# Performance work log

Hardware: AMD Instinct MI355X
Metric: run time of the kernel (lower is better)

## Reference

```python
import jax, jax.numpy as jnp
import numpy as np

B, T = 16384, 79
DIMS = [(1, 64), (64, 32), (32, 16), (16, 8), (8, 16), (16, 32), (32, 64), (64, 79)]


def _simple_rnn(x, Wx, Wh, b, act, return_seq):
    # x: [B, T, D] -> SimpleRNN: h_t = act(x_t @ Wx + h_{t-1} @ Wh + b)
    xb = jnp.einsum('btd,du->btu', x, Wx) + b  # precompute input projection
    h0 = jnp.zeros((x.shape[0], Wh.shape[0]), x.dtype)

    def step(h, xt):
        h = act(xt + h @ Wh)
        return h, h

    hT, hs = jax.lax.scan(step, h0, jnp.swapaxes(xb, 0, 1))  # scan over time
    return jnp.swapaxes(hs, 0, 1) if return_seq else hT


def setup_inputs() -> dict:
    key = jax.random.key(0)
    ks = jax.random.split(key, 3 * len(DIMS) + 1)
    inp = {"x": jax.random.normal(ks[0], (B, T), dtype=jnp.float32)}
    for i, (d, u) in enumerate(DIMS):
        inp[f"Wx{i}"] = jax.random.normal(ks[1 + 3 * i], (d, u), dtype=jnp.float32) / np.sqrt(d).astype(np.float32)
        inp[f"Wh{i}"] = jax.random.normal(ks[2 + 3 * i], (u, u), dtype=jnp.float32) / np.sqrt(u).astype(np.float32)
        inp[f"b{i}"] = jnp.zeros((u,), dtype=jnp.float32)
    return inp


def reference(x, Wx0, Wh0, b0, Wx1, Wh1, b1, Wx2, Wh2, b2, Wx3, Wh3, b3,
              Wx4, Wh4, b4, Wx5, Wh5, b5, Wx6, Wh6, b6, Wx7, Wh7, b7):
    params = [(Wx0, Wh0, b0), (Wx1, Wh1, b1), (Wx2, Wh2, b2), (Wx3, Wh3, b3),
              (Wx4, Wh4, b4), (Wx5, Wh5, b5), (Wx6, Wh6, b6), (Wx7, Wh7, b7)]
    h = x[..., None]  # [B, T, 1]  (tf.expand_dims(x, -1))
    n = len(params)
    for i, (Wx, Wh, b) in enumerate(params):
        last = i == n - 1
        act = jax.nn.sigmoid if last else jax.nn.relu
        h = _simple_rnn(h, Wx, Wh, b, act, return_seq=not last)
    return h  # decoded: [B, 79]
```

## Files before the change

kernel.cpp:

```cpp
#include <hip/hip_runtime.h>
#include <hip/hip_bf16.h>

#define DEVFN static __device__ __forceinline__

typedef short bf16x8 __attribute__((ext_vector_type(8)));
typedef float f32x4  __attribute__((ext_vector_type(4)));

constexpr int TSEQ  = 79;
constexpr int NSTEP = TSEQ + 7;
constexpr int MWG   = 16;
constexpr int ROWU  = 344;
constexpr int NBLK  = 16384 / MWG;

constexpr int LD[8]   = {1,64,32,16,8,16,32,64};
constexpr int LU[8]   = {64,32,16,8,16,32,64,79};
constexpr int LS[8]   = {0,8,72,104,120,128,144,176};
constexpr int LO[8]   = {8,72,104,120,128,144,176,240};
constexpr int LKP[8]  = {96,96,64,32,32,64,96,160};
constexpr int LKS[8]  = {3,3,2,1,1,2,3,5};
constexpr int LUP[8]  = {64,32,16,16,16,32,64,80};
constexpr int WOFF[8] = {0,6144,9216,10240,10752,11264,13312,19456};
constexpr int WTOTAL  = 32256;

constexpr int WNG[4]     = {1,2,4,2};
constexpr int WGL[4][4]  = {{7,0,0,0},{7,1,0,0},{0,2,3,4},{6,5,0,0}};
constexpr int WGT0[4][4] = {{0,0,0,0},{3,0,0,0},{0,0,0,0},{0,0,0,0}};
constexpr int WGNT[4][4] = {{3,0,0,0},{2,2,0,0},{4,1,1,1},{4,2,0,0}};

DEVFN unsigned short f2bf(float f) {
  unsigned int u = __builtin_bit_cast(unsigned int, f);
  return (unsigned short)((u + 0x7FFFu + ((u >> 16) & 1u)) >> 16);
}
DEVFN unsigned int pk_rna(float a, float b) {
  unsigned int ua = __builtin_bit_cast(unsigned int, a) + 0x8000u;
  unsigned int ub = __builtin_bit_cast(unsigned int, b) + 0x8000u;
  return __builtin_amdgcn_perm(ub, ua, 0x07060302u);
}
DEVFN float sigmoidf(float v) {
  return __builtin_amdgcn_rcpf(1.0f + __expf(-v));
}

__global__ void __launch_bounds__(256) prep_weights(
    const float* Wx0, const float* Wh0, const float* Wx1, const float* Wh1,
    const float* Wx2, const float* Wh2, const float* Wx3, const float* Wh3,
    const float* Wx4, const float* Wh4, const float* Wx5, const float* Wh5,
    const float* Wx6, const float* Wh6, const float* Wx7, const float* Wh7,
    unsigned short* __restrict__ wt)
{
  const float* wxp[8] = {Wx0,Wx1,Wx2,Wx3,Wx4,Wx5,Wx6,Wx7};
  const float* whp[8] = {Wh0,Wh1,Wh2,Wh3,Wh4,Wh5,Wh6,Wh7};
  int idx = blockIdx.x * 256 + threadIdx.x;
  if (idx >= WTOTAL) return;
#pragma unroll
  for (int l = 0; l < 8; ++l) {
    int sz = LUP[l] * LKP[l];
    if (idx >= WOFF[l] && idx < WOFF[l] + sz) {
      int local = idx - WOFF[l];
      int j = local / LKP[l];
      int k = local - j * LKP[l];
      float v = 0.f;
      if (j < LU[l]) {
        if (l == 0) {
          if (k == 0) v = Wx0[j];
          else if (k >= 8 && k < 72) v = Wh0[(k - 8) * 64 + j];
        } else {
          if (k < LD[l]) v = wxp[l][k * LU[l] + j];
          else if (k < LD[l] + LU[l]) v = whp[l][(k - LD[l]) * LU[l] + j];
        }
      }
      wt[idx] = f2bf(v);
    }
  }
}

template <int W>
DEVFN void preload(const unsigned short* __restrict__ wt,
                   const float* const (&bptr)[8], int lane,
                   bf16x8 (&af)[16], f32x4 (&bi)[7])
{
  const int m0 = lane & 15, quad = lane >> 4;
  int ai = 0, ti = 0;
#pragma unroll
  for (int g = 0; g < 4; ++g) {
    if (g >= WNG[W]) break;
    const int l = WGL[W][g], t0 = WGT0[W][g], nt = WGNT[W][g];
    const int ks = LKS[l], Kp = LKP[l], u = LU[l];
#pragma unroll
    for (int t = 0; t < 4; ++t) {
      if (t >= nt) continue;
      const int j = (t0 + t) * 16 + m0;
      const unsigned short* base = wt + WOFF[l] + j * Kp;
#pragma unroll
      for (int k = 0; k < 5; ++k) {
        if (k >= ks) continue;
        af[ai + t * ks + k] = *reinterpret_cast<const bf16x8*>(base + k * 32 + quad * 8);
      }
      const float* bp = bptr[l];
      f32x4 bv;
#pragma unroll
      for (int r = 0; r < 4; ++r) {
        int j2 = (t0 + t) * 16 + quad * 4 + r;
        bv[r] = (j2 < u) ? bp[j2] : 0.0f;
      }
      bi[ti + t] = bv;
    }
    ai += nt * ks; ti += nt;
  }
}

template <int W>
DEVFN void step(int s, const unsigned short (&rb)[MWG][ROWU], unsigned short (&wb)[MWG][ROWU],
                const bf16x8 (&af)[16], const f32x4 (&bi)[7],
                const unsigned short (*xl)[80], float* __restrict__ out,
                int bb, int lane)
{
  const int m = lane & 15, quad = lane >> 4;
  int ai = 0, ti = 0;
#pragma unroll
  for (int g = 0; g < 4; ++g) {
    if (g >= WNG[W]) break;
    const int l = WGL[W][g], t0 = WGT0[W][g], nt = WGNT[W][g];
    const int ks = LKS[l], S = LS[l], O = LO[l], u = LU[l];
    if (s >= l && s <= l + TSEQ - 1) {
      f32x4 acc[4];
#pragma unroll
      for (int k = 0; k < 5; ++k) {
        if (k >= ks) break;
        bf16x8 bfv = *reinterpret_cast<const bf16x8*>(&rb[m][S + k * 32 + quad * 8]);
#pragma unroll
        for (int t = 0; t < 4; ++t)
          if (t < nt)
            acc[t] = __builtin_amdgcn_mfma_f32_16x16x32_bf16(
                af[ai + t * ks + k], bfv, (k == 0) ? bi[ti + t] : acc[t], 0, 0, 0);
      }
#pragma unroll
      for (int t = 0; t < 4; ++t) {
        if (t >= nt) continue;
        const int jb = (t0 + t) * 16 + quad * 4;
        float v0 = acc[t][0], v1 = acc[t][1], v2 = acc[t][2], v3 = acc[t][3];
        if (l == 7) {
          v0 = sigmoidf(v0); v1 = sigmoidf(v1); v2 = sigmoidf(v2); v3 = sigmoidf(v3);
          if (s == NSTEP - 1) {
            float* op = out + (size_t)(bb + m) * 79 + jb;
            if (jb + 0 < 79) op[0] = v0;
            if (jb + 1 < 79) op[1] = v1;
            if (jb + 2 < 79) op[2] = v2;
            if (jb + 3 < 79) op[3] = v3;
          } else {
            uint2 pk;
            pk.x = pk_rna(v0, v1);
            pk.y = pk_rna(v2, v3);
            *reinterpret_cast<uint2*>(&wb[m][O + jb]) = pk;
          }
        } else {
          if (jb < u) {
            v0 = fmaxf(v0, 0.f); v1 = fmaxf(v1, 0.f); v2 = fmaxf(v2, 0.f); v3 = fmaxf(v3, 0.f);
            uint2 pk;
            pk.x = pk_rna(v0, v1);
            pk.y = pk_rna(v2, v3);
            *reinterpret_cast<uint2*>(&wb[m][O + jb]) = pk;
          }
        }
      }
    }
    ai += nt * ks; ti += nt;
  }
  if constexpr (W == 0) {
    if (lane < MWG && s < TSEQ - 1) {
      wb[lane][0] = xl[lane][s + 1];
    }
  }
}

__global__ void __launch_bounds__(256)
__attribute__((amdgpu_waves_per_eu(4, 4)))
__attribute__((amdgpu_num_vgpr(128)))
rnn_wavefront(
    const float* __restrict__ x, const unsigned short* __restrict__ wt,
    const float* b0, const float* b1, const float* b2, const float* b3,
    const float* b4, const float* b5, const float* b6, const float* b7,
    float* __restrict__ out)
{
  __shared__ __align__(16) unsigned short hb0[MWG][ROWU];
  __shared__ __align__(16) unsigned short hb1[MWG][ROWU];
  __shared__ __align__(4)  unsigned short xl[MWG][80];
  const int tid = threadIdx.x, lane = tid & 63, wid = tid >> 6;
  const int bb = blockIdx.x * MWG;
  const float* bptr[8] = {b0, b1, b2, b3, b4, b5, b6, b7};

  {
    unsigned int* p0 = (unsigned int*)&hb0[0][0];
    unsigned int* p1 = (unsigned int*)&hb1[0][0];
    constexpr int NW = MWG * ROWU / 2;
    for (int i = tid; i < NW; i += 256) { p0[i] = 0; p1[i] = 0; }
  }
  {
    const float* xb = x + (size_t)bb * TSEQ;
    for (int i = tid; i < MWG * TSEQ; i += 256) {
      int r = i / TSEQ, c = i - r * TSEQ;
      xl[r][c] = f2bf(xb[i]);
    }
  }
  __syncthreads();
  if (tid < MWG) hb0[tid][0] = xl[tid][0];

  bf16x8 af[16];
  f32x4  bi[7];
  if (wid == 0)      preload<0>(wt, bptr, lane, af, bi);
  else if (wid == 1) preload<1>(wt, bptr, lane, af, bi);
  else if (wid == 2) preload<2>(wt, bptr, lane, af, bi);
  else               preload<3>(wt, bptr, lane, af, bi);
  __syncthreads();

#pragma unroll 1
  for (int s = 0; s < NSTEP; s += 2) {
    if (wid == 0)      step<0>(s, hb0, hb1, af, bi, xl, out, bb, lane);
    else if (wid == 1) step<1>(s, hb0, hb1, af, bi, xl, out, bb, lane);
    else if (wid == 2) step<2>(s, hb0, hb1, af, bi, xl, out, bb, lane);
    else               step<3>(s, hb0, hb1, af, bi, xl, out, bb, lane);
    __syncthreads();
    if (wid == 0)      step<0>(s + 1, hb1, hb0, af, bi, xl, out, bb, lane);
    else if (wid == 1) step<1>(s + 1, hb1, hb0, af, bi, xl, out, bb, lane);
    else if (wid == 2) step<2>(s + 1, hb1, hb0, af, bi, xl, out, bb, lane);
    else               step<3>(s + 1, hb1, hb0, af, bi, xl, out, bb, lane);
    __syncthreads();
  }
}

extern "C" void kernel_launch(void* const* d_in, const int* in_sizes, int n_in,
                              void* d_out, int out_size, void* d_ws, size_t ws_size,
                              hipStream_t stream)
{
  const float* x = (const float*)d_in[0];
  const float* Wx[8]; const float* Wh[8]; const float* b[8];
  for (int i = 0; i < 8; ++i) {
    Wx[i] = (const float*)d_in[1 + 3 * i];
    Wh[i] = (const float*)d_in[2 + 3 * i];
    b[i]  = (const float*)d_in[3 + 3 * i];
  }
  unsigned short* wt = (unsigned short*)d_ws;

  prep_weights<<<(WTOTAL + 255) / 256, 256, 0, stream>>>(
      Wx[0], Wh[0], Wx[1], Wh[1], Wx[2], Wh[2], Wx[3], Wh[3],
      Wx[4], Wh[4], Wx[5], Wh[5], Wx[6], Wh[6], Wx[7], Wh[7], wt);

  rnn_wavefront<<<NBLK, 256, 0, stream>>>(
      x, wt, b[0], b[1], b[2], b[3], b[4], b[5], b[6], b[7], (float*)d_out);
}
```

Measured before the change: 206.3 us.

## Run all eight RNN layers per wave with register-resident weights

Replaces the layer-wavefront schedule, where four waves each owned some layers and synchronised through block barriers on double-buffered LDS, with a scheme where each wave processes a private 16-row batch tile through all eight layers sequentially per timestep. All layer weights (63 bf16x8 fragments) and biases stay in registers, and occupancy drops to one wave per EU. Intra-wave LDS fences replace __syncthreads, and hidden-state fragments from the previous step are preloaded before the layer chain. This removes barrier stalls and cross-wave dependencies but raises register pressure and lowers latency hiding from occupancy. The serial per-wave dependency chain across eight layers may also expose MFMA and LDS latency.

```diff
diff --git a/kernel.cpp b/kernel.cpp
--- a/kernel.cpp
+++ b/kernel.cpp
@@ -7,10 +7,9 @@
 typedef float f32x4  __attribute__((ext_vector_type(4)));
 
 constexpr int TSEQ  = 79;
-constexpr int NSTEP = TSEQ + 7;
 constexpr int MWG   = 16;
 constexpr int ROWU  = 344;
-constexpr int NBLK  = 16384 / MWG;
+constexpr int NBLK  = 16384 / 64;
 
 constexpr int LD[8]   = {1,64,32,16,8,16,32,64};
 constexpr int LU[8]   = {64,32,16,8,16,32,64,79};
@@ -22,10 +21,14 @@
 constexpr int WOFF[8] = {0,6144,9216,10240,10752,11264,13312,19456};
 constexpr int WTOTAL  = 32256;
 
-constexpr int WNG[4]     = {1,2,4,2};
-constexpr int WGL[4][4]  = {{7,0,0,0},{7,1,0,0},{0,2,3,4},{6,5,0,0}};
-constexpr int WGT0[4][4] = {{0,0,0,0},{3,0,0,0},{0,0,0,0},{0,0,0,0}};
-constexpr int WGNT[4][4] = {{3,0,0,0},{2,2,0,0},{4,1,1,1},{4,2,0,0}};
+constexpr int NT[8]  = {4,2,1,1,1,2,4,5};
+constexpr int AO[8]  = {0,12,18,20,21,22,26,38};
+constexpr int TO[8]  = {0,4,6,7,8,9,11,15};
+constexpr int NH[8]  = {3,1,1,0,0,1,2,3};
+constexpr int BHO[8] = {0,3,4,5,5,5,6,8};
+constexpr int KORD[8][5] = {
+  {0,1,2,0,0},{2,0,1,0,0},{1,0,0,0,0},{0,0,0,0,0},
+  {0,0,0,0,0},{1,0,0,0,0},{1,2,0,0,0},{2,3,4,0,1}};
 
 DEVFN unsigned short f2bf(float f) {
   unsigned int u = __builtin_bit_cast(unsigned int, f);
@@ -38,6 +41,12 @@
 }
 DEVFN float sigmoidf(float v) {
   return __builtin_amdgcn_rcpf(1.0f + __expf(-v));
+}
+
+DEVFN void ds_fence() {
+  __builtin_amdgcn_sched_barrier(0);
+  asm volatile("s_waitcnt lgkmcnt(0)" ::: "memory");
+  __builtin_amdgcn_sched_barrier(0);
 }
 
 __global__ void __launch_bounds__(256) prep_weights(
@@ -73,158 +82,170 @@
   }
 }
 
-template <int W>
-DEVFN void preload(const unsigned short* __restrict__ wt,
-                   const float* const (&bptr)[8], int lane,
-                   bf16x8 (&af)[16], f32x4 (&bi)[7])
+DEVFN void preload_all(const unsigned short* __restrict__ wt,
+                       const float* const (&bptr)[8], int lane,
+                       bf16x8 (&af)[63], f32x4 (&bi)[20])
 {
   const int m0 = lane & 15, quad = lane >> 4;
-  int ai = 0, ti = 0;
-#pragma unroll
-  for (int g = 0; g < 4; ++g) {
-    if (g >= WNG[W]) break;
-    const int l = WGL[W][g], t0 = WGT0[W][g], nt = WGNT[W][g];
-    const int ks = LKS[l], Kp = LKP[l], u = LU[l];
-#pragma unroll
-    for (int t = 0; t < 4; ++t) {
-      if (t >= nt) continue;
-      const int j = (t0 + t) * 16 + m0;
-      const unsigned short* base = wt + WOFF[l] + j * Kp;
+#pragma unroll
+  for (int l = 0; l < 8; ++l) {
+#pragma unroll
+    for (int t = 0; t < 5; ++t) {
+      if (t >= NT[l]) continue;
+      const unsigned short* base = wt + WOFF[l] + (t * 16 + m0) * LKP[l];
 #pragma unroll
       for (int k = 0; k < 5; ++k) {
-        if (k >= ks) continue;
-        af[ai + t * ks + k] = *reinterpret_cast<const bf16x8*>(base + k * 32 + quad * 8);
+        if (k >= LKS[l]) continue;
+        af[AO[l] + t * LKS[l] + k] =
+            *reinterpret_cast<const bf16x8*>(base + k * 32 + quad * 8);
       }
       const float* bp = bptr[l];
       f32x4 bv;
 #pragma unroll
       for (int r = 0; r < 4; ++r) {
-        int j2 = (t0 + t) * 16 + quad * 4 + r;
-        bv[r] = (j2 < u) ? bp[j2] : 0.0f;
-      }
-      bi[ti + t] = bv;
-    }
-    ai += nt * ks; ti += nt;
-  }
-}
-
-template <int W>
-DEVFN void step(int s, const unsigned short (&rb)[MWG][ROWU], unsigned short (&wb)[MWG][ROWU],
-                const bf16x8 (&af)[16], const f32x4 (&bi)[7],
-                const unsigned short (*xl)[80], float* __restrict__ out,
-                int bb, int lane)
+        int j2 = t * 16 + quad * 4 + r;
+        bv[r] = (j2 < LU[l]) ? bp[j2] : 0.0f;
+      }
+      bi[TO[l] + t] = bv;
+    }
+  }
+}
+
+template <int L, bool LAST>
+DEVFN void layer(const unsigned short* rbase,
+                 unsigned short* wbase,
+                 const bf16x8 (&af)[63], const f32x4 (&bi)[20],
+                 const bf16x8 (&bh)[11],
+                 float* __restrict__ out, int bb, int m, int quad)
+{
+  constexpr int ks = LKS[L], nt = NT[L], S = LS[L], O = LO[L], u = LU[L];
+  bf16x8 fr[5];
+#pragma unroll
+  for (int i = 0; i < 5; ++i) {
+    if (i < NH[L] || i >= ks) continue;
+    fr[i] = *reinterpret_cast<const bf16x8*>(rbase + S + KORD[L][i] * 32);
+  }
+  f32x4 acc[5];
+#pragma unroll
+  for (int i = 0; i < 5; ++i) {
+    if (i >= ks) continue;
+    bf16x8 b = (i < NH[L]) ? bh[BHO[L] + i] : fr[i];
+#pragma unroll
+    for (int t = 0; t < 5; ++t) {
+      if (t >= nt) continue;
+      acc[t] = __builtin_amdgcn_mfma_f32_16x16x32_bf16(
+          af[AO[L] + t * ks + KORD[L][i]], b,
+          (i == 0) ? bi[TO[L] + t] : acc[t], 0, 0, 0);
+    }
+  }
+#pragma unroll
+  for (int t = 0; t < 5; ++t) {
+    if (t >= nt) continue;
+    const int jb = t * 16 + quad * 4;
+    float v0 = acc[t][0], v1 = acc[t][1], v2 = acc[t][2], v3 = acc[t][3];
+    if (L == 7) {
+      v0 = sigmoidf(v0); v1 = sigmoidf(v1); v2 = sigmoidf(v2); v3 = sigmoidf(v3);
+      if (LAST) {
+        float* op = out + (size_t)(bb + m) * 79 + jb;
+        if (jb + 0 < 79) op[0] = v0;
+        if (jb + 1 < 79) op[1] = v1;
+        if (jb + 2 < 79) op[2] = v2;
+        if (jb + 3 < 79) op[3] = v3;
+      } else {
+        uint2 pk;
+        pk.x = pk_rna(v0, v1);
+        pk.y = pk_rna(v2, v3);
+        *reinterpret_cast<uint2*>(wbase + O + t * 16) = pk;
+      }
+    } else {
+      if (jb < u) {
+        v0 = fmaxf(v0, 0.f); v1 = fmaxf(v1, 0.f); v2 = fmaxf(v2, 0.f); v3 = fmaxf(v3, 0.f);
+        uint2 pk;
+        pk.x = pk_rna(v0, v1);
+        pk.y = pk_rna(v2, v3);
+        *reinterpret_cast<uint2*>(wbase + O + t * 16) = pk;
+      }
+    }
+  }
+}
+
+template <bool LAST>
+DEVFN void timestep(int t, unsigned short (&hw)[MWG][ROWU],
+                    const unsigned short (&xw)[MWG][80],
+                    const bf16x8 (&af)[63], const f32x4 (&bi)[20],
+                    float* __restrict__ out, int bb, int lane)
 {
   const int m = lane & 15, quad = lane >> 4;
-  int ai = 0, ti = 0;
-#pragma unroll
-  for (int g = 0; g < 4; ++g) {
-    if (g >= WNG[W]) break;
-    const int l = WGL[W][g], t0 = WGT0[W][g], nt = WGNT[W][g];
-    const int ks = LKS[l], S = LS[l], O = LO[l], u = LU[l];
-    if (s >= l && s <= l + TSEQ - 1) {
-      f32x4 acc[4];
-#pragma unroll
-      for (int k = 0; k < 5; ++k) {
-        if (k >= ks) break;
-        bf16x8 bfv = *reinterpret_cast<const bf16x8*>(&rb[m][S + k * 32 + quad * 8]);
-#pragma unroll
-        for (int t = 0; t < 4; ++t)
-          if (t < nt)
-            acc[t] = __builtin_amdgcn_mfma_f32_16x16x32_bf16(
-                af[ai + t * ks + k], bfv, (k == 0) ? bi[ti + t] : acc[t], 0, 0, 0);
-      }
-#pragma unroll
-      for (int t = 0; t < 4; ++t) {
-        if (t >= nt) continue;
-        const int jb = (t0 + t) * 16 + quad * 4;
-        float v0 = acc[t][0], v1 = acc[t][1], v2 = acc[t][2], v3 = acc[t][3];
-        if (l == 7) {
-          v0 = sigmoidf(v0); v1 = sigmoidf(v1); v2 = sigmoidf(v2); v3 = sigmoidf(v3);
-          if (s == NSTEP - 1) {
-            float* op = out + (size_t)(bb + m) * 79 + jb;
-            if (jb + 0 < 79) op[0] = v0;
-            if (jb + 1 < 79) op[1] = v1;
-            if (jb + 2 < 79) op[2] = v2;
-            if (jb + 3 < 79) op[3] = v3;
-          } else {
-            uint2 pk;
-            pk.x = pk_rna(v0, v1);
-            pk.y = pk_rna(v2, v3);
-            *reinterpret_cast<uint2*>(&wb[m][O + jb]) = pk;
-          }
-        } else {
-          if (jb < u) {
-            v0 = fmaxf(v0, 0.f); v1 = fmaxf(v1, 0.f); v2 = fmaxf(v2, 0.f); v3 = fmaxf(v3, 0.f);
-            uint2 pk;
-            pk.x = pk_rna(v0, v1);
-            pk.y = pk_rna(v2, v3);
-            *reinterpret_cast<uint2*>(&wb[m][O + jb]) = pk;
-          }
-        }
-      }
-    }
-    ai += nt * ks; ti += nt;
-  }
-  if constexpr (W == 0) {
-    if (lane < MWG && s < TSEQ - 1) {
-      wb[lane][0] = xl[lane][s + 1];
-    }
-  }
+  const unsigned short* rbase = &hw[m][quad * 8];
+  unsigned short* wbase = &hw[m][quad * 4];
+  if (lane < MWG) hw[lane][0] = xw[lane][t];
+  ds_fence();
+  bf16x8 bh[11];
+#pragma unroll
+  for (int l = 0; l < 8; ++l) {
+#pragma unroll
+    for (int i = 0; i < 3; ++i) {
+      if (i >= NH[l]) continue;
+      bh[BHO[l] + i] =
+          *reinterpret_cast<const bf16x8*>(rbase + LS[l] + KORD[l][i] * 32);
+    }
+  }
+  ds_fence();
+  layer<0, LAST>(rbase, wbase, af, bi, bh, out, bb, m, quad);
+  ds_fence();
+  layer<1, LAST>(rbase, wbase, af, bi, bh, out, bb, m, quad);
+  ds_fence();
+  layer<2, LAST>(rbase, wbase, af, bi, bh, out, bb, m, quad);
+  ds_fence();
+  layer<3, LAST>(rbase, wbase, af, bi, bh, out, bb, m, quad);
+  ds_fence();
+  layer<4, LAST>(rbase, wbase, af, bi, bh, out, bb, m, quad);
+  ds_fence();
+  layer<5, LAST>(rbase, wbase, af, bi, bh, out, bb, m, quad);
+  ds_fence();
+  layer<6, LAST>(rbase, wbase, af, bi, bh, out, bb, m, quad);
+  ds_fence();
+  layer<7, LAST>(rbase, wbase, af, bi, bh, out, bb, m, quad);
+  ds_fence();
 }
 
 __global__ void __launch_bounds__(256)
-__attribute__((amdgpu_waves_per_eu(4, 4)))
-__attribute__((amdgpu_num_vgpr(128)))
-rnn_wavefront(
-    const float* __restrict__ x, const unsigned short* __restrict__ wt,
-    const float* b0, const float* b1, const float* b2, const float* b3,
-    const float* b4, const float* b5, const float* b6, const float* b7,
-    float* __restrict__ out)
-{
-  __shared__ __align__(16) unsigned short hb0[MWG][ROWU];
-  __shared__ __align__(16) unsigned short hb1[MWG][ROWU];
-  __shared__ __align__(4)  unsigned short xl[MWG][80];
+__attribute__((amdgpu_waves_per_eu(1, 1)))
+rnn_reg(const float* __restrict__ x, const unsigned short* __restrict__ wt,
+        const float* b0, const float* b1, const float* b2, const float* b3,
+        const float* b4, const float* b5, const float* b6, const float* b7,
+        float* __restrict__ out)
+{
+  __shared__ __align__(16) unsigned short hb[4][MWG][ROWU];
+  __shared__ __align__(4)  unsigned short xl[4][MWG][80];
   const int tid = threadIdx.x, lane = tid & 63, wid = tid >> 6;
-  const int bb = blockIdx.x * MWG;
+  const int bb = blockIdx.x * 64 + wid * MWG;
   const float* bptr[8] = {b0, b1, b2, b3, b4, b5, b6, b7};
 
   {
-    unsigned int* p0 = (unsigned int*)&hb0[0][0];
-    unsigned int* p1 = (unsigned int*)&hb1[0][0];
-    constexpr int NW = MWG * ROWU / 2;
-    for (int i = tid; i < NW; i += 256) { p0[i] = 0; p1[i] = 0; }
+    unsigned int* p = (unsigned int*)&hb[0][0][0];
+    constexpr int NW = 4 * MWG * ROWU / 2;
+    for (int i = tid; i < NW; i += 256) p[i] = 0;
   }
   {
-    const float* xb = x + (size_t)bb * TSEQ;
-    for (int i = tid; i < MWG * TSEQ; i += 256) {
+    const float* xb = x + (size_t)blockIdx.x * 64 * TSEQ;
+    for (int i = tid; i < 64 * TSEQ; i += 256) {
       int r = i / TSEQ, c = i - r * TSEQ;
-      xl[r][c] = f2bf(xb[i]);
-    }
-  }
+      xl[r >> 4][r & 15][c] = f2bf(xb[i]);
+    }
+  }
+  bf16x8 af[63];
+  f32x4  bi[20];
+  preload_all(wt, bptr, lane, af, bi);
   __syncthreads();
-  if (tid < MWG) hb0[tid][0] = xl[tid][0];
-
-  bf16x8 af[16];
-  f32x4  bi[7];
-  if (wid == 0)      preload<0>(wt, bptr, lane, af, bi);
-  else if (wid == 1) preload<1>(wt, bptr, lane, af, bi);
-  else if (wid == 2) preload<2>(wt, bptr, lane, af, bi);
-  else               preload<3>(wt, bptr, lane, af, bi);
-  __syncthreads();
+
+  unsigned short (&hw)[MWG][ROWU] = hb[wid];
+  const unsigned short (&xw)[MWG][80] = xl[wid];
 
 #pragma unroll 1
-  for (int s = 0; s < NSTEP; s += 2) {
-    if (wid == 0)      step<0>(s, hb0, hb1, af, bi, xl, out, bb, lane);
-    else if (wid == 1) step<1>(s, hb0, hb1, af, bi, xl, out, bb, lane);
-    else if (wid == 2) step<2>(s, hb0, hb1, af, bi, xl, out, bb, lane);
-    else               step<3>(s, hb0, hb1, af, bi, xl, out, bb, lane);
-    __syncthreads();
-    if (wid == 0)      step<0>(s + 1, hb1, hb0, af, bi, xl, out, bb, lane);
-    else if (wid == 1) step<1>(s + 1, hb1, hb0, af, bi, xl, out, bb, lane);
-    else if (wid == 2) step<2>(s + 1, hb1, hb0, af, bi, xl, out, bb, lane);
-    else               step<3>(s + 1, hb1, hb0, af, bi, xl, out, bb, lane);
-    __syncthreads();
-  }
+  for (int t = 0; t < TSEQ - 1; ++t)
+    timestep<false>(t, hw, xw, af, bi, out, bb, lane);
+  timestep<true>(TSEQ - 1, hw, xw, af, bi, out, bb, lane);
 }
 
 extern "C" void kernel_launch(void* const* d_in, const int* in_sizes, int n_in,
@@ -244,6 +265,6 @@
       Wx[0], Wh[0], Wx[1], Wh[1], Wx[2], Wh[2], Wx[3], Wh[3],
       Wx[4], Wh[4], Wx[5], Wh[5], Wx[6], Wh[6], Wx[7], Wh[7], wt);
 
-  rnn_wavefront<<<NBLK, 256, 0, stream>>>(
+  rnn_reg<<<NBLK, 256, 0, stream>>>(
       x, wt, b[0], b[1], b[2], b[3], b[4], b[5], b[6], b[7], (float*)d_out);
 }
```

After: 259.3 us. 1.26x slower.
